# Performance work log

Measured on AMD Instinct MI355X. Metric: run time of the kernel, lower is better.

## Reference

```python
import jax, jax.numpy as jnp
import numpy as np

D = 128          # embedding_size
K = 8            # num_components
S = 65536        # seq_len
SCALE = 1.0 / np.sqrt(2.0 * np.pi)  # keeps det(2*pi*Sigma) and exp(-maha/2) in fp32 range


def setup_inputs() -> dict:
    key = jax.random.key(0)
    kx, kw, kb = jax.random.split(key, 3)
    x = jax.random.normal(kx, (1, S, D), dtype=jnp.float32) * SCALE
    W = jax.random.normal(kw, (D, K), dtype=jnp.float32) / np.sqrt(D)
    b = jax.random.normal(kb, (K,), dtype=jnp.float32) * 0.01
    return {"x": x, "W": W, "b": b}


def reference(x, W, b):
    xs = x[0]                                    # [S, D]  (x.squeeze())
    seq_len = xs.shape[0]
    # component responsibilities: Linear + Softmax
    gamma = jax.nn.softmax(xs @ W + b, axis=-1)  # [S, K]
    Nk = jnp.sum(gamma, axis=0)                  # [K]   sum of component weights
    phi = Nk / seq_len                           # [K]   mixture weights (component_weight_)
    # per-component means: sum_j gamma_jk x_j / Nk
    mu = (gamma.T @ xs) / Nk[:, None]            # [K, D]
    diff = xs[:, None, :] - mu[None, :, :]       # [S, K, D]
    # per-component covariance: sum_j gamma_jk (x_j-mu_k)(x_j-mu_k)^T / Nk
    sigma = jnp.einsum('sk,skd,ske->kde', gamma, diff, diff) / Nk[:, None, None]  # [K, D, D]
    inv_sigma = jnp.linalg.inv(sigma)            # [K, D, D]
    # Mahalanobis distance per (sample, component)
    maha = jnp.einsum('skd,kde,ske->sk', diff, inv_sigma, diff)  # [S, K]
    two_pi = jnp.float32(2.0 * np.pi)
    det = jnp.abs(jnp.linalg.det(two_pi * sigma))                # [K]  det(2*pi*Sigma_k)
    dens = jnp.sum(phi * jnp.exp(-0.5 * maha) / jnp.sqrt(det), axis=-1)  # [S]
    energy = -jnp.sum(jnp.log(dens))
    return energy.reshape(1, 1)
```

## Files before the change

kernel.cpp:

```cpp
#include <hip/hip_runtime.h>


#define S_LEN 65536
#define D 128
#define K 8
#define NCH 32
#define KSTEP 64
#define NXTCH (S_LEN / KSTEP)
#define MB_S 128
#define NMB (S_LEN / MB_S)

#define OFF_GT 0
#define SZ_GT (NXTCH * K * KSTEP)
#define OFF_M2P (OFF_GT + SZ_GT)
#define SZ_M2P (K * NCH * D * D)
#define OFF_MSP (OFF_M2P + SZ_M2P)
#define SZ_MSP (K * NCH * D)
#define OFF_NKP (OFF_MSP + SZ_MSP)
#define SZ_NKP (K * NCH)
#define OFF_NK (OFF_NKP + SZ_NKP)
#define OFF_MU (OFF_NK + 8)
#define OFF_SIGMA (OFF_MU + K * D)
#define OFF_WV (OFF_SIGMA + K * D * D)
#define OFF_COEF (OFF_WV + K * D)
#define OFF_C2 (OFF_COEF + 8)
#define OFF_EPART (OFF_C2 + 8)
#define OFF_XB (OFF_EPART + NMB)
#define SZ_XB (S_LEN * D / 2)
#define OFF_XT (OFF_XB + SZ_XB)
#define SZ_XT (S_LEN * D / 2)
#define OFF_BH (OFF_XT + SZ_XT)

#define LOG_2PI 1.8378770664093453f

typedef __attribute__((ext_vector_type(8))) short short8;
typedef __attribute__((ext_vector_type(4))) float f32x4;

__device__ __forceinline__ float bflo(unsigned u) { return __uint_as_float(u << 16); }
__device__ __forceinline__ float bfhi(unsigned u) { return __uint_as_float(u & 0xffff0000u); }
__device__ __forceinline__ float bfu(unsigned short u) { return __uint_as_float((unsigned)u << 16); }
__device__ __forceinline__ unsigned packbf(float a, float b) {
  unsigned ua = __float_as_uint(a); ua = ua + 0x7fffu + ((ua >> 16) & 1);
  unsigned ub = __float_as_uint(b); ub = ub + 0x7fffu + ((ub >> 16) & 1);
  return (ua >> 16) | (ub & 0xffff0000u);
}

__global__ __launch_bounds__(256) void k_gamma(const float* __restrict__ x,
                                               const float* __restrict__ W,
                                               const float* __restrict__ b,
                                               float* __restrict__ gt) {
  __shared__ float Wt[K][D];
  __shared__ float bl[K];
  int tid = threadIdx.x;
  for (int it = 0; it < 4; ++it) {
    int idx = it * 256 + tid;
    Wt[idx & 7][idx >> 3] = W[idx];
  }
  if (tid < K) bl[tid] = b[tid];
  __syncthreads();

  int s = blockIdx.x * 256 + tid;
  float li[K];
#pragma unroll
  for (int k = 0; k < K; ++k) li[k] = bl[k];
  const float4* xr = (const float4*)(x + (size_t)s * D);
#pragma unroll 8
  for (int i = 0; i < 32; ++i) {
    float4 xv = xr[i];
#pragma unroll
    for (int k = 0; k < K; ++k) {
      float4 wv = *(const float4*)&Wt[k][i * 4];
      li[k] += xv.x * wv.x + xv.y * wv.y + xv.z * wv.z + xv.w * wv.w;
    }
  }
  float m = li[0];
#pragma unroll
  for (int k = 1; k < K; ++k) m = fmaxf(m, li[k]);
  float p[K];
  float sum = 0.f;
#pragma unroll
  for (int k = 0; k < K; ++k) { p[k] = expf(li[k] - m); sum += p[k]; }
  float inv = 1.0f / sum;
  int ch = s >> 6, sl = s & 63;
#pragma unroll
  for (int k = 0; k < K; ++k) gt[(size_t)ch * (K * 64) + k * 64 + sl] = p[k] * inv;
}

__global__ __launch_bounds__(256) void k_xprep(const float* __restrict__ x,
                                               unsigned short* __restrict__ xb,
                                               unsigned short* __restrict__ xt) {
  __shared__ unsigned short xr[64 * 136];
  int tid = threadIdx.x;
  for (int c = 0; c < 4; ++c) {
    int sb = blockIdx.x * 256 + c * 64;
    if (c) __syncthreads();
    {
      int s = tid >> 2, db = (tid & 3) * 32;
      const float4* src = (const float4*)(x + (size_t)(sb + s) * D + db);
#pragma unroll
      for (int j = 0; j < 4; ++j) {
        float4 v0 = src[j * 2], v1 = src[j * 2 + 1];
        unsigned u0 = packbf(v0.x, v0.y), u1 = packbf(v0.z, v0.w);
        unsigned u2 = packbf(v1.x, v1.y), u3 = packbf(v1.z, v1.w);
        uint4 o = {u0, u1, u2, u3};
        *(uint4*)&xr[s * 136 + db + j * 8] = o;
      }
    }
    __syncthreads();
    {
      int s = tid >> 2, u0 = (tid & 3) * 4;
      uint4* dst = (uint4*)(xb + (size_t)(sb + s) * D) + u0;
#pragma unroll
      for (int j = 0; j < 4; ++j) dst[j] = *(const uint4*)&xr[s * 136 + (u0 + j) * 8];
    }
    {
      int d = tid >> 1, lu0 = (tid & 1) * 4;
      uint4* dst = (uint4*)(xt + (size_t)(sb >> 6) * (D * 64) + d * 64) + lu0;
#pragma unroll
      for (int j = 0; j < 4; ++j) {
        int s0 = (lu0 + j) * 8;
        unsigned w[4];
#pragma unroll
        for (int q = 0; q < 4; ++q) {
          unsigned lo = xr[(s0 + 2 * q) * 136 + d];
          unsigned hi = xr[(s0 + 2 * q + 1) * 136 + d];
          w[q] = lo | (hi << 16);
        }
        uint4 o = {w[0], w[1], w[2], w[3]};
        dst[j] = o;
      }
    }
  }
}

__global__ __launch_bounds__(256) void k_m2(const unsigned short* __restrict__ xt,
                                            const float* __restrict__ gt,
                                            float* __restrict__ m2p,
                                            float* __restrict__ msp,
                                            float* __restrict__ nkp) {
  __shared__ unsigned short zt[D * 64];
  __shared__ float gbuf[2][64], sgbuf[2][64];
  __shared__ float msred[256];
  int tid = threadIdx.x;
  int cblk = blockIdx.x, k = blockIdx.y;
  int ch0 = cblk * 32;

  int w = tid >> 6;
  int m0 = (w >> 1) * 64, n0 = (w & 1) * 64;
  int lg = (tid >> 4) & 3, ll = tid & 15;

  const uint4* xtg = (const uint4*)xt;
  uint4 xr[4];
  {
    const uint4* src = xtg + (size_t)ch0 * 1024 + tid * 4;
#pragma unroll
    for (int j = 0; j < 4; ++j) xr[j] = src[j];
  }
  float gacc = 0.f, gn = 0.f;
  if (tid < 64) {
    float g0 = gt[(size_t)ch0 * (K * 64) + k * 64 + tid];
    gbuf[0][tid] = g0; sgbuf[0][tid] = sqrtf(g0); gacc = g0;
    gn = gt[(size_t)(ch0 + 1) * (K * 64) + k * 64 + tid];
  }
  __syncthreads();

  f32x4 acc[4][4];
#pragma unroll
  for (int mi = 0; mi < 4; ++mi)
#pragma unroll
    for (int ni = 0; ni < 4; ++ni) acc[mi][ni] = (f32x4)0.f;

  float msa = 0.f;
  int dloc = tid >> 1;

  for (int t = 0; t < 32; ++t) {
    int cur = t & 1;
#pragma unroll
    for (int j = 0; j < 4; ++j) {
      int lu = (tid & 1) * 4 + j, s0 = lu * 8;
      uint4 q = xr[j];
      float x0 = bflo(q.x), x1 = bfhi(q.x), x2 = bflo(q.y), x3 = bfhi(q.y);
      float x4 = bflo(q.z), x5 = bfhi(q.z), x6 = bflo(q.w), x7 = bfhi(q.w);
      float4 g0 = *(const float4*)&gbuf[cur][s0];
      float4 g1 = *(const float4*)&gbuf[cur][s0 + 4];
      float4 s0v = *(const float4*)&sgbuf[cur][s0];
      float4 s1v = *(const float4*)&sgbuf[cur][s0 + 4];
      msa += x0 * g0.x + x1 * g0.y + x2 * g0.z + x3 * g0.w +
             x4 * g1.x + x5 * g1.y + x6 * g1.z + x7 * g1.w;
      unsigned u0 = packbf(x0 * s0v.x, x1 * s0v.y);
      unsigned u1 = packbf(x2 * s0v.z, x3 * s0v.w);
      unsigned u2 = packbf(x4 * s1v.x, x5 * s1v.y);
      unsigned u3 = packbf(x6 * s1v.z, x7 * s1v.w);
      uint4 o = {u0, u1, u2, u3};
      *(uint4*)&zt[dloc * 64 + (lu ^ (dloc & 7)) * 8] = o;
    }
    if (tid < 64 && t + 1 < 32) {
      gbuf[cur ^ 1][tid] = gn; sgbuf[cur ^ 1][tid] = sqrtf(gn); gacc += gn;
    }
    if (t + 1 < 32) {
      const uint4* src = xtg + (size_t)(ch0 + t + 1) * 1024 + tid * 4;
#pragma unroll
      for (int j = 0; j < 4; ++j) xr[j] = src[j];
      if (tid < 64 && t + 2 < 32)
        gn = gt[(size_t)(ch0 + t + 2) * (K * 64) + k * 64 + tid];
    }
    __syncthreads();
#pragma unroll
    for (int ksub = 0; ksub < 2; ++ksub) {
      short8 af[4], bf_[4];
#pragma unroll
      for (int mi = 0; mi < 4; ++mi) {
        int dd = m0 + mi * 16 + ll;
        int ua = ksub * 4 + lg;
        af[mi] = *(const short8*)&zt[dd * 64 + (ua ^ (dd & 7)) * 8];
      }
#pragma unroll
      for (int ni = 0; ni < 4; ++ni) {
        int ee = n0 + ni * 16 + ll;
        int ub = ksub * 4 + lg;
        bf_[ni] = *(const short8*)&zt[ee * 64 + (ub ^ (ee & 7)) * 8];
      }
#pragma unroll
      for (int mi = 0; mi < 4; ++mi)
#pragma unroll
        for (int ni = 0; ni < 4; ++ni)
          acc[mi][ni] = __builtin_amdgcn_mfma_f32_16x16x32_bf16(
              af[mi], bf_[ni], acc[mi][ni], 0, 0, 0);
    }
    __syncthreads();
  }

  size_t base = (size_t)(k * NCH + cblk) << 14;
#pragma unroll
  for (int mi = 0; mi < 4; ++mi)
#pragma unroll
    for (int ni = 0; ni < 4; ++ni)
#pragma unroll
      for (int r = 0; r < 4; ++r) {
        int row = m0 + mi * 16 + lg * 4 + r;
        int col = n0 + ni * 16 + ll;
        m2p[base + row * D + col] = acc[mi][ni][r];
      }
  msred[tid] = msa;
  __syncthreads();
  if (tid < 128) msp[(size_t)(k * NCH + cblk) * D + tid] = msred[2 * tid] + msred[2 * tid + 1];
  if (tid < 64) {
    float v = gacc;
#pragma unroll
    for (int off = 1; off < 64; off <<= 1) v += __shfl_xor(v, off);
    if (tid == 0) nkp[k * NCH + cblk] = v;
  }
}

__global__ __launch_bounds__(256) void k_redmu(const float* __restrict__ msp,
                                               const float* __restrict__ nkp,
                                               float* __restrict__ Nk,
                                               float* __restrict__ mu) {
  __shared__ float sNk[K];
  int tid = threadIdx.x;
  if (tid < K) {
    float s = 0.f;
    for (int c = 0; c < NCH; ++c) s += nkp[tid * NCH + c];
    sNk[tid] = s;
    Nk[tid] = s;
  }
  __syncthreads();
  for (int it = 0; it < (K * D) / 256; ++it) {
    int idx = it * 256 + tid;
    int k = idx >> 7;
    float s = 0.f;
    for (int c = 0; c < NCH; ++c) s += msp[(size_t)(k * NCH + c) * D + (idx & 127)];
    mu[idx] = s / sNk[k];
  }
}

__global__ __launch_bounds__(256) void k_sigma(const float* __restrict__ m2p,
                                               const float* __restrict__ Nk,
                                               const float* __restrict__ mu,
                                               float* __restrict__ sigma) {
  int tid = threadIdx.x;
  int k = blockIdx.y;
  int flat = blockIdx.x * 256 + tid;
  int d = flat >> 7, e = flat & 127;
  float s = 0.f;
  for (int c = 0; c < NCH; ++c) s += m2p[((size_t)(k * NCH + c) << 14) + flat];
  sigma[((size_t)k << 14) + flat] = s / Nk[k] - mu[k * D + d] * mu[k * D + e];
}

#define PBW 36
#define YTW 132
#define AROT(r, c) (((r) << 7) + ((((c) + (((r) >> 3) << 2))) & 127))

__global__ __launch_bounds__(256) void k_inv(const float* __restrict__ sigma,
                                             const float* __restrict__ Nk,
                                             const float* __restrict__ mu,
                                             unsigned short* __restrict__ Bh,
                                             float* __restrict__ vv,
                                             float* __restrict__ coef,
                                             float* __restrict__ c2) {
  __shared__ float A[D * D];
  __shared__ float Pb[32 * PBW];
  __shared__ float Cb[32 * 128];
  __shared__ float Yt[32 * YTW];
  __shared__ float Rb[32 * 128];
  __shared__ float mus[D];
  int tid = threadIdx.x;
  int k = blockIdx.x;
  const float* sg = sigma + ((size_t)k << 14);

#pragma unroll
  for (int i = 0; i < 16; ++i) {
    int f = tid + 256 * i;
    int r = f >> 5, c4 = (f & 31) << 2;
    *(float4*)&A[AROT(r, c4)] = *(const float4*)&sg[((size_t)f) << 2];
  }
  if (tid < D) mus[tid] = mu[k * D + tid];
  __syncthreads();

  float ldet = 0.f;
  int mr = tid >> 3, mq = tid & 7;
  int ci = tid >> 1, ch = tid & 1;
  int w = tid >> 6, l = tid & 63;
  int d0 = (((w >> 1) << 3) + (l >> 3)) * 8;
  int e0 = (((w & 1) << 3) + (l & 7)) * 8;

  for (int t = 0; t < 4; ++t) {
    int tb = t * 32;
    *(float4*)&Pb[mr * PBW + 4 * mq] = *(const float4*)&A[AROT(tb + mr, tb + 4 * mq)];
#pragma unroll
    for (int q = 0; q < 4; ++q) {
      int f = tid + 256 * q;
      int rr = f >> 5, cc4 = (f & 31) << 2;
      *(float4*)&Rb[rr * 128 + cc4] = *(const float4*)&A[AROT(tb + rr, cc4)];
    }
#pragma unroll
    for (int n4 = 0; n4 < 4; ++n4) {
      float4 q4 = *(const float4*)&A[AROT(ci, tb + 16 * ch + 4 * n4)];
      int nb = 16 * ch + 4 * n4;
      Cb[(nb + 0) * 128 + ci] = q4.x;
      Cb[(nb + 1) * 128 + ci] = q4.y;
      Cb[(nb + 2) * 128 + ci] = q4.z;
      Cb[(nb + 3) * 128 + ci] = q4.w;
    }
    __syncthreads();

    for (int c = 0; c < 32; ++c) {
      float dpv = Pb[c * PBW + c];
      float piv = 1.0f / dpv;
      ldet += logf(dpv);
      float4 rq = *(const float4*)&Pb[c * PBW + 4 * mq];
      float cv = Pb[mr * PBW + c];
      __syncthreads();
      float4 rfac = {piv * rq.x, piv * rq.y, piv * rq.z, piv * rq.w};
      float4 own = *(const float4*)&Pb[mr * PBW + 4 * mq];
      bool pr = (mr == c);
      float4 up;
      up.x = pr ? rfac.x : own.x - cv * rfac.x;
      up.y = pr ? rfac.y : own.y - cv * rfac.y;
      up.z = pr ? rfac.z : own.z - cv * rfac.z;
      up.w = pr ? rfac.w : own.w - cv * rfac.w;
      int cq = c >> 2, cl = c & 3;
      if (mq == cq) {
        float nv = pr ? -piv : cv * piv;
        if (cl == 0) up.x = nv;
        else if (cl == 1) up.y = nv;
        else if (cl == 2) up.z = nv;
        else up.w = nv;
      }
      *(float4*)&Pb[mr * PBW + 4 * mq] = up;
      __syncthreads();
    }

    {
      int rs = tid >> 3, cs = tid & 7;
      float accY[4][4] = {};
#pragma unroll 8
      for (int n = 0; n < 32; ++n) {
        float4 cq4 = *(const float4*)&Cb[n * 128 + 4 * rs];
        float4 pq = *(const float4*)&Pb[n * PBW + 4 * cs];
        float ca[4] = {cq4.x, cq4.y, cq4.z, cq4.w};
        float pa[4] = {pq.x, pq.y, pq.z, pq.w};
#pragma unroll
        for (int q = 0; q < 4; ++q)
#pragma unroll
          for (int j = 0; j < 4; ++j) accY[q][j] -= ca[q] * pa[j];
      }
#pragma unroll
      for (int j = 0; j < 4; ++j) {
        float4 o = {accY[0][j], accY[1][j], accY[2][j], accY[3][j]};
        *(float4*)&Yt[(4 * cs + j) * YTW + 4 * rs] = o;
      }
    }
    __syncthreads();

    {
      float acc[8][8];
#pragma unroll
      for (int di = 0; di < 8; ++di)
#pragma unroll
        for (int e4 = 0; e4 < 2; ++e4) {
          float4 a = *(const float4*)&A[AROT(d0 + di, e0 + 4 * e4)];
          acc[di][e4 * 4 + 0] = a.x; acc[di][e4 * 4 + 1] = a.y;
          acc[di][e4 * 4 + 2] = a.z; acc[di][e4 * 4 + 3] = a.w;
        }
#pragma unroll 4
      for (int m = 0; m < 32; ++m) {
        float4 ya = *(const float4*)&Yt[m * YTW + d0];
        float4 yb = *(const float4*)&Yt[m * YTW + d0 + 4];
        float4 ra = *(const float4*)&Rb[m * 128 + e0];
        float4 rb2 = *(const float4*)&Rb[m * 128 + e0 + 4];
        float av[8] = {ya.x, ya.y, ya.z, ya.w, yb.x, yb.y, yb.z, yb.w};
        float bv[8] = {ra.x, ra.y, ra.z, ra.w, rb2.x, rb2.y, rb2.z, rb2.w};
#pragma unroll
        for (int di = 0; di < 8; ++di)
#pragma unroll
          for (int ei = 0; ei < 8; ++ei) acc[di][ei] -= av[di] * bv[ei];
      }
#pragma unroll
      for (int di = 0; di < 8; ++di)
#pragma unroll
        for (int e4 = 0; e4 < 2; ++e4) {
          float4 o = {acc[di][e4 * 4 + 0], acc[di][e4 * 4 + 1],
                      acc[di][e4 * 4 + 2], acc[di][e4 * 4 + 3]};
          *(float4*)&A[AROT(d0 + di, e0 + 4 * e4)] = o;
        }
    }
    __syncthreads();

#pragma unroll
    for (int qq = 0; qq < 4; ++qq) {
      int j0 = 4 * mq + 32 * qq;
      *(float4*)&A[AROT(tb + mr, j0)] = *(const float4*)&Yt[mr * YTW + j0];
    }
    if (ci < tb || ci >= tb + 32) {
#pragma unroll
      for (int n = 0; n < 16; ++n) {
        int mloc = 16 * ch + ((n + ci) & 15);
        A[AROT(ci, tb + mloc)] = Yt[mloc * YTW + ci];
      }
    }
    __syncthreads();
    *(float4*)&A[AROT(tb + mr, tb + 4 * mq)] = *(const float4*)&Pb[mr * PBW + 4 * mq];
    __syncthreads();
  }

#pragma unroll
  for (int i = 0; i < 16; ++i) {
    int f = tid + 256 * i;
    int r = f >> 5, c4 = (f & 31) << 2;
    float4 a = *(const float4*)&A[AROT(r, c4)];
    unsigned u0 = packbf(-a.x, -a.y), u1 = packbf(-a.z, -a.w);
    uint2 o = {u0, u1};
    *(uint2*)(Bh + (size_t)k * (D * D) + f * 4) = o;
  }
  float c2part = 0.f;
  if (tid < D) {
    float s = 0.f;
#pragma unroll 8
    for (int q = 0; q < 32; ++q) {
      float4 a = *(const float4*)&A[AROT(tid, q << 2)];
      float4 m = *(const float4*)&mus[q << 2];
      s += a.x * m.x + a.y * m.y + a.z * m.z + a.w * m.w;
    }
    vv[k * D + tid] = -s;
    c2part = mus[tid] * (-s);
  }
  __syncthreads();
  {
    float v = c2part;
#pragma unroll
    for (int off = 1; off < 64; off <<= 1) v += __shfl_xor(v, off);
    if ((tid & 63) == 0) Pb[tid >> 6] = v;
  }
  __syncthreads();
  if (tid == 0) {
    c2[k] = Pb[0] + Pb[1];
    coef[k] = logf(Nk[k] * (1.0f / (float)S_LEN)) -
              0.5f * ((float)D * LOG_2PI + ldet);
  }
}

__global__ __launch_bounds__(256) void k_maha(const unsigned short* __restrict__ xb,
                                              const unsigned short* __restrict__ Bh,
                                              const float* __restrict__ vv,
                                              const float* __restrict__ coef,
                                              const float* __restrict__ c2,
                                              float* __restrict__ epart) {
  __shared__ unsigned short Bt[D * D];
  __shared__ float vls[K * D];
  __shared__ float cfl[K], c2l[K];
  __shared__ float wsum[4];
  int tid = threadIdx.x;
  int bs = blockIdx.x * MB_S;
  int w = tid >> 6, l = tid & 63;
  int m0 = w * 32;
  int lg = (tid >> 4) & 3, ll = tid & 15;

  short8 af[2][4];
#pragma unroll
  for (int mi = 0; mi < 2; ++mi) {
    const unsigned short* rp = xb + (size_t)(bs + m0 + mi * 16 + ll) * D;
#pragma unroll
    for (int jj = 0; jj < 4; ++jj)
      af[mi][jj] = *(const short8*)(rp + jj * 32 + lg * 8);
  }
  unsigned short ex[2][4][8];
#pragma unroll
  for (int mi = 0; mi < 2; ++mi)
#pragma unroll
    for (int r = 0; r < 4; ++r) {
      const unsigned short* rp = xb + (size_t)(bs + m0 + mi * 16 + lg * 4 + r) * D + ll;
#pragma unroll
      for (int ni = 0; ni < 8; ++ni) ex[mi][r][ni] = rp[ni * 16];
    }

#pragma unroll
  for (int i = 0; i < 4; ++i) { int idx = i * 256 + tid; vls[idx] = vv[idx]; }
  if (tid < K) { cfl[tid] = coef[tid]; c2l[tid] = c2[tid]; }

  const uint4* bg = (const uint4*)Bh;
  uint4 br[8];
#pragma unroll
  for (int j = 0; j < 8; ++j) br[j] = bg[j * 256 + tid];

  float mrun[2][4], srun[2][4];
#pragma unroll
  for (int mi = 0; mi < 2; ++mi)
#pragma unroll
    for (int r = 0; r < 4; ++r) { mrun[mi][r] = -1e30f; srun[mi][r] = 0.f; }

  for (int k = 0; k < K; ++k) {
#pragma unroll
    for (int j = 0; j < 8; ++j) {
      int u = j * 256 + tid;
      int e = u >> 4, du = u & 15;
      *(uint4*)&Bt[e * D + ((du ^ (e & 7)) << 3)] = br[j];
    }
    if (k + 1 < K) {
      const uint4* src = bg + (size_t)(k + 1) * 2048;
#pragma unroll
      for (int j = 0; j < 8; ++j) br[j] = src[j * 256 + tid];
    }
    __syncthreads();

    f32x4 acc[2][8];
#pragma unroll
    for (int mi = 0; mi < 2; ++mi)
#pragma unroll
      for (int ni = 0; ni < 8; ++ni) acc[mi][ni] = (f32x4)0.f;
#pragma unroll
    for (int jj = 0; jj < 4; ++jj) {
#pragma unroll
      for (int ni = 0; ni < 8; ++ni) {
        int e = ni * 16 + ll;
        int du = jj * 4 + lg;
        short8 bfr = *(const short8*)&Bt[e * D + ((du ^ (e & 7)) << 3)];
#pragma unroll
        for (int mi = 0; mi < 2; ++mi)
          acc[mi][ni] = __builtin_amdgcn_mfma_f32_16x16x32_bf16(
              af[mi][jj], bfr, acc[mi][ni], 0, 0, 0);
      }
    }

    float part[2][4] = {};
#pragma unroll
    for (int ni = 0; ni < 8; ++ni) {
      int col = ni * 16 + ll;
      float w2 = -2.0f * vls[k * D + col];
#pragma unroll
      for (int mi = 0; mi < 2; ++mi)
#pragma unroll
        for (int r = 0; r < 4; ++r)
          part[mi][r] += bfu(ex[mi][r][ni]) * (acc[mi][ni][r] + w2);
    }
#pragma unroll
    for (int mi = 0; mi < 2; ++mi)
#pragma unroll
      for (int r = 0; r < 4; ++r) {
        float p = part[mi][r];
        p += __shfl_xor(p, 1); p += __shfl_xor(p, 2);
        p += __shfl_xor(p, 4); p += __shfl_xor(p, 8);
        float a = cfl[k] - 0.5f * (p + c2l[k]);
        float mn = fmaxf(mrun[mi][r], a);
        srun[mi][r] = srun[mi][r] * expf(mrun[mi][r] - mn) + expf(a - mn);
        mrun[mi][r] = mn;
      }
    __syncthreads();
  }

  float v = 0.f;
#pragma unroll
  for (int mi = 0; mi < 2; ++mi)
#pragma unroll
    for (int r = 0; r < 4; ++r) v += mrun[mi][r] + logf(srun[mi][r]);
  v += __shfl_xor(v, 16);
  v += __shfl_xor(v, 32);
  if (l == 0) wsum[w] = v;
  __syncthreads();
  if (tid == 0) epart[blockIdx.x] = wsum[0] + wsum[1] + wsum[2] + wsum[3];
}

__global__ __launch_bounds__(256) void k_final(const float* __restrict__ epart,
                                               float* __restrict__ out) {
  __shared__ double sw[4];
  int tid = threadIdx.x;
  double a = (double)epart[tid] + (double)epart[tid + 256];
#pragma unroll
  for (int off = 1; off < 64; off <<= 1) a += __shfl_xor(a, off);
  if ((tid & 63) == 0) sw[tid >> 6] = a;
  __syncthreads();
  if (tid == 0) out[0] = (float)(-(sw[0] + sw[1] + sw[2] + sw[3]));
}

extern "C" void kernel_launch(void* const* d_in, const int* in_sizes, int n_in,
                              void* d_out, int out_size, void* d_ws, size_t ws_size,
                              hipStream_t stream) {
  (void)in_sizes; (void)n_in; (void)out_size; (void)ws_size;
  const float* x = (const float*)d_in[0];
  const float* W = (const float*)d_in[1];
  const float* b = (const float*)d_in[2];
  float* out = (float*)d_out;
  float* ws = (float*)d_ws;

  float* gtp   = ws + OFF_GT;
  float* m2p   = ws + OFF_M2P;
  float* msp   = ws + OFF_MSP;
  float* nkp   = ws + OFF_NKP;
  float* Nk    = ws + OFF_NK;
  float* mu    = ws + OFF_MU;
  float* sigma = ws + OFF_SIGMA;
  float* wvp   = ws + OFF_WV;
  float* coefp = ws + OFF_COEF;
  float* c2p   = ws + OFF_C2;
  float* epart = ws + OFF_EPART;
  unsigned short* xb = (unsigned short*)(ws + OFF_XB);
  unsigned short* xt = (unsigned short*)(ws + OFF_XT);
  unsigned short* Bh = (unsigned short*)(ws + OFF_BH);

  k_gamma<<<S_LEN / 256, 256, 0, stream>>>(x, W, b, gtp);
  k_xprep<<<S_LEN / 256, 256, 0, stream>>>(x, xb, xt);
  k_m2<<<dim3(NCH, K), 256, 0, stream>>>(xt, gtp, m2p, msp, nkp);
  k_redmu<<<1, 256, 0, stream>>>(msp, nkp, Nk, mu);
  k_sigma<<<dim3(64, K), 256, 0, stream>>>(m2p, Nk, mu, sigma);
  k_inv<<<K, 256, 0, stream>>>(sigma, Nk, mu, Bh, wvp, coefp, c2p);
  k_maha<<<NMB, 256, 0, stream>>>(xb, Bh, wvp, coefp, c2p, epart);
  k_final<<<1, 256, 0, stream>>>(epart, out);
}
```

Measured before the change: 298.7 us.

## Run 32x32 pivot-block Gauss-Jordan inverse in a single wavefront

The in-place Gauss-Jordan inversion of each 32x32 diagonal pivot block now runs inside wave 0 only, with each lane owning half a row (16 elements). This replaces two block-wide __syncthreads per pivot step with wavefront-level barriers, removing synchronisation across all 256 threads in the serial elimination loop. The cost is less parallelism per step (64 lanes each doing 16 elements instead of 256 threads doing 4), while the other waves sit idle until a final block barrier. Correctness relies on wave-synchronous execution within wave 0 and on variables w and l being defined earlier in the kernel.

```diff
diff --git a/kernel.cpp b/kernel.cpp
--- a/kernel.cpp
+++ b/kernel.cpp
@@ -290,6 +290,14 @@
 #define PBW 36
 #define YTW 132
 #define AROT(r, c) (((r) << 7) + ((((c) + (((r) >> 3) << 2))) & 127))
+#define SWQ(o, p) { f32x4 rf_; rf_[0] = piv * (p).x; rf_[1] = piv * (p).y;      \
+  rf_[2] = piv * (p).z; rf_[3] = piv * (p).w;                                   \
+  (o).x = prw ? rf_[0] : (o).x - cv * rf_[0];                                   \
+  (o).y = prw ? rf_[1] : (o).y - cv * rf_[1];                                   \
+  (o).z = prw ? rf_[2] : (o).z - cv * rf_[2];                                   \
+  (o).w = prw ? rf_[3] : (o).w - cv * rf_[3]; }
+#define SETL(q) { if (cl == 0) (q).x = nv; else if (cl == 1) (q).y = nv;        \
+  else if (cl == 2) (q).z = nv; else (q).w = nv; }
 
 __global__ __launch_bounds__(256) void k_inv(const float* __restrict__ sigma,
                                              const float* __restrict__ Nk,
@@ -344,32 +352,43 @@
     }
     __syncthreads();
 
-    for (int c = 0; c < 32; ++c) {
-      float dpv = Pb[c * PBW + c];
-      float piv = 1.0f / dpv;
-      ldet += logf(dpv);
-      float4 rq = *(const float4*)&Pb[c * PBW + 4 * mq];
-      float cv = Pb[mr * PBW + c];
-      __syncthreads();
-      float4 rfac = {piv * rq.x, piv * rq.y, piv * rq.z, piv * rq.w};
-      float4 own = *(const float4*)&Pb[mr * PBW + 4 * mq];
-      bool pr = (mr == c);
-      float4 up;
-      up.x = pr ? rfac.x : own.x - cv * rfac.x;
-      up.y = pr ? rfac.y : own.y - cv * rfac.y;
-      up.z = pr ? rfac.z : own.z - cv * rfac.z;
-      up.w = pr ? rfac.w : own.w - cv * rfac.w;
-      int cq = c >> 2, cl = c & 3;
-      if (mq == cq) {
-        float nv = pr ? -piv : cv * piv;
-        if (cl == 0) up.x = nv;
-        else if (cl == 1) up.y = nv;
-        else if (cl == 2) up.z = nv;
-        else up.w = nv;
-      }
-      *(float4*)&Pb[mr * PBW + 4 * mq] = up;
-      __syncthreads();
-    }
+    if (w == 0) {
+      int rr = l >> 1, h = l & 1;
+      float* own = &Pb[rr * PBW + h * 16];
+      const int hb = h * 16;
+      for (int c = 0; c < 32; ++c) {
+        float dpv = Pb[c * PBW + c];
+        float piv = 1.0f / dpv;
+        ldet += logf(dpv);
+        const float* prow = &Pb[c * PBW + hb];
+        float4 p0 = *(const float4*)&prow[0];
+        float4 p1 = *(const float4*)&prow[4];
+        float4 p2 = *(const float4*)&prow[8];
+        float4 p3 = *(const float4*)&prow[12];
+        float cv = Pb[rr * PBW + c];
+        float4 o0 = *(const float4*)&own[0];
+        float4 o1 = *(const float4*)&own[4];
+        float4 o2 = *(const float4*)&own[8];
+        float4 o3 = *(const float4*)&own[12];
+        __builtin_amdgcn_wave_barrier();
+        bool prw = (rr == c);
+        SWQ(o0, p0) SWQ(o1, p1) SWQ(o2, p2) SWQ(o3, p3)
+        if ((c >> 4) == h) {
+          float nv = prw ? -piv : cv * piv;
+          int cq = (c >> 2) & 3, cl = c & 3;
+          if (cq == 0) SETL(o0)
+          else if (cq == 1) SETL(o1)
+          else if (cq == 2) SETL(o2)
+          else SETL(o3)
+        }
+        *(float4*)&own[0] = o0;
+        *(float4*)&own[4] = o1;
+        *(float4*)&own[8] = o2;
+        *(float4*)&own[12] = o3;
+        __builtin_amdgcn_wave_barrier();
+      }
+    }
+    __syncthreads();
 
     {
       int rs = tid >> 3, cs = tid & 7;
```

New measurement: 302.0 us. Within noise of the previous version (+1.1%).
